# Kernel tuning notes

Hardware: AMD Instinct MI355X
Metric: run time of the kernel (lower is better)

## Reference

```python
import jax, jax.numpy as jnp
import numpy as np

C = 64
CQ = C // 8


def setup_inputs() -> dict:
    key = jax.random.key(0)
    ks = jax.random.split(key, 8)
    x = jax.random.normal(ks[0], (8, C, 64, 64), dtype=jnp.float32)
    s = 1.0 / np.sqrt(C)
    Wq = jax.random.normal(ks[1], (CQ, C), dtype=jnp.float32) * s
    bq = jax.random.normal(ks[2], (CQ,), dtype=jnp.float32) * s
    Wk = jax.random.normal(ks[3], (CQ, C), dtype=jnp.float32) * s
    bk = jax.random.normal(ks[4], (CQ,), dtype=jnp.float32) * s
    Wv = jax.random.normal(ks[5], (C, C), dtype=jnp.float32) * s
    bv = jax.random.normal(ks[6], (C,), dtype=jnp.float32) * s
    gamma = jnp.array([0.5], dtype=jnp.float32)  # nonzero so value path contributes
    return {"x": x, "Wq": Wq, "bq": bq, "Wk": Wk, "bk": bk, "Wv": Wv, "bv": bv, "gamma": gamma}


def reference(x, Wq, bq, Wk, bk, Wv, bv, gamma):
    B, Cc, H, W = x.shape
    xf = x.reshape(B, Cc, H * W)  # [B, C, N]
    # 1x1 conv == channel-mixing linear
    f = jnp.einsum('oc,bcn->bon', Wq, xf) + bq[None, :, None]  # [B, C/8, N]
    g = jnp.einsum('oc,bcn->bon', Wk, xf) + bk[None, :, None]  # [B, C/8, N]
    h = jnp.einsum('oc,bcn->bon', Wv, xf) + bv[None, :, None]  # [B, C, N]
    # scores[b,i,j] = f[b,:,i] . g[b,:,j]; softmax over dim=1 (query dim i)
    scores = jnp.einsum('bdi,bdj->bij', f, g)  # [B, N, N]
    beta = jax.nn.softmax(scores, axis=1)
    o = gamma[0] * jnp.einsum('bcn,bnm->bcm', h, beta) + xf
    return o.reshape(B, Cc, H, W)
```

## Files before the change

### kernel.cpp

```cpp
#include <hip/hip_runtime.h>
#include <hip/hip_fp16.h>


typedef _Float16 half8_t __attribute__((ext_vector_type(8)));
typedef _Float16 half4_t __attribute__((ext_vector_type(4)));
typedef _Float16 half2_t __attribute__((ext_vector_type(2)));
typedef __fp16  fp16x2  __attribute__((ext_vector_type(2)));
typedef float float4_t __attribute__((ext_vector_type(4)));

#define NTOK 4096
#define PRH 72
#define LOG2E 1.44269504088896340736f

#if __has_builtin(__builtin_amdgcn_exp2f)
__device__ __forceinline__ float fexp2(float x) { return __builtin_amdgcn_exp2f(x); }
#else
__device__ __forceinline__ float fexp2(float x) { return exp2f(x); }
#endif

__device__ __forceinline__ half2_t pkcvt(float a, float b) {
    fp16x2 v = __builtin_amdgcn_cvt_pkrtz(a, b);
    return __builtin_bit_cast(half2_t, v);
}

__global__ __launch_bounds__(320) void proj_kernel(
    const float* __restrict__ x,
    const float* __restrict__ Wq, const float* __restrict__ bq,
    const float* __restrict__ Wk, const float* __restrict__ bk,
    const float* __restrict__ Wv, const float* __restrict__ bv,
    __half* __restrict__ fTR, __half* __restrict__ gT16, __half* __restrict__ hM)
{
    __shared__ float xl[64 * 64];
    const int t  = threadIdx.x;
    const int kt = blockIdx.x;
    const int b  = blockIdx.y;
    const int n0 = kt * 64;

    if (t < 256) {
        const int f4 = t & 15;
        const int cb = t >> 4;
#pragma unroll
        for (int i = 0; i < 4; i++) {
            const int c = cb + i * 16;
            float4 v = *(const float4*)(x + (((size_t)(b * 64 + c)) << 12) + n0 + f4 * 4);
            *(float4*)(&xl[c * 64 + f4 * 4]) = v;
        }
    }
    __syncthreads();

    const int w    = t >> 6;
    const int lane = t & 63;
    const int n    = n0 + lane;
    float acc[16];

    if (w == 0) {
#pragma unroll
        for (int j = 0; j < 8; j++) { acc[j] = bq[j]; acc[8 + j] = bk[j]; }
        float xc = xl[lane];
        for (int c = 0; c < 64; c++) {
            const float xn = (c < 63) ? xl[(c + 1) * 64 + lane] : 0.f;
#pragma unroll
            for (int j = 0; j < 8; j++) {
                acc[j]     += Wq[j * 64 + c] * xc;
                acc[8 + j] += Wk[j * 64 + c] * xc;
            }
            xc = xn;
        }
        float gn2 = 0.f;
#pragma unroll
        for (int j = 0; j < 8; j++) gn2 += acc[8 + j] * acc[8 + j];
        const float M = (LOG2E * 4.6f) * __builtin_sqrtf(gn2) + 1.0f;

        const int t4 = lane >> 4, ml = lane & 15;
        half4_t flo = {(_Float16)(acc[0] * LOG2E), (_Float16)(acc[1] * LOG2E),
                       (_Float16)(acc[2] * LOG2E), (_Float16)(acc[3] * LOG2E)};
        half4_t fhi = {(_Float16)(acc[4] * LOG2E), (_Float16)(acc[5] * LOG2E),
                       (_Float16)(acc[6] * LOG2E), (_Float16)(acc[7] * LOG2E)};
        __half* fb = fTR + ((size_t)b << 15) + (size_t)(kt * 16 + ml) * 32 + t4 * 4;
        *(half4_t*)fb        = flo;
        *(half4_t*)(fb + 16) = fhi;

        half8_t glo, gpad;
#pragma unroll
        for (int j = 0; j < 8; j++) glo[j] = (_Float16)acc[8 + j];
        gpad = (half8_t){};
        gpad[0] = (_Float16)(-M);
        __half* gp = gT16 + (size_t)((b << 12) + n) * 16;
        *(half8_t*)gp       = glo;
        *(half8_t*)(gp + 8) = gpad;
    } else {
        const int ch0 = (w - 1) * 16;
#pragma unroll
        for (int j = 0; j < 16; j++) acc[j] = bv[ch0 + j];
        float xc = xl[lane];
        for (int c = 0; c < 64; c++) {
            const float xn = (c < 63) ? xl[(c + 1) * 64 + lane] : 0.f;
#pragma unroll
            for (int j = 0; j < 16; j++) acc[j] += Wv[(ch0 + j) * 64 + c] * xc;
            xc = xn;
        }
#pragma unroll
        for (int j = 0; j < 16; j++)
            hM[(((size_t)b * 64 + ch0 + j) << 12) + n] = __float2half(acc[j]);
    }
}

template<int NT>
__global__ __launch_bounds__(256) void attn_kernel(
    const __half* __restrict__ fTR, const __half* __restrict__ gT16,
    const __half* __restrict__ hM,
    __half* __restrict__ Pacc, float* __restrict__ Lsum)
{
    __shared__ __align__(16) _Float16 hl[2][64 * PRH];
    const int tid   = threadIdx.x;
    const int w     = tid >> 6;
    const int lane  = tid & 63;
    const int q     = lane >> 4;
    const int ml    = lane & 15;
    const int b     = blockIdx.y;
    const int split = blockIdx.z;
    const int colA  = blockIdx.x * 128 + w * 16 + ml;
    const int colB  = colA + 64;
    const bool qlo  = (q < 2);

    half4_t gfA = *(const half4_t*)(gT16 + ((size_t)((b << 12) + colA)) * 16 + q * 4);
    half4_t gfB = *(const half4_t*)(gT16 + ((size_t)((b << 12) + colB)) * 16 + q * 4);

    float4_t accA[4], accB[4];
#pragma unroll
    for (int cg = 0; cg < 4; cg++) {
        accA[cg] = (float4_t){0.f, 0.f, 0.f, 0.f};
        accB[cg] = (float4_t){0.f, 0.f, 0.f, 0.f};
    }
    float lsA0 = 0.f, lsA1 = 0.f, lsA2 = 0.f, lsA3 = 0.f;
    float lsB0 = 0.f, lsB1 = 0.f, lsB2 = 0.f, lsB3 = 0.f;

    const int kt0 = split * NT;
    const int c0  = tid >> 3;
    const int g0  = tid & 7;

    const __half* srow0 = hM + ((size_t)(b * 64 + c0) << 12) + kt0 * 64 + g0 * 8;
    const __half* srow1 = srow0 + ((size_t)32 << 12);
    const __half* fptr  = fTR + ((size_t)b << 15) + (size_t)(kt0 * 16 + ml) * 32 + q * 16;

    half4_t padv = (half4_t){};
    if (q == 2) padv[0] = (_Float16)1.0f;

    uint4 s0 = *(const uint4*)srow0;
    uint4 s1 = *(const uint4*)srow1;
    half4_t afn0 = padv, afn1 = padv, afn2 = padv, afn3 = padv;
    if (qlo) {
        afn0 = *(const half4_t*)(fptr);
        afn1 = *(const half4_t*)(fptr + 4);
        afn2 = *(const half4_t*)(fptr + 8);
        afn3 = *(const half4_t*)(fptr + 12);
    }
    *(uint4*)(&hl[0][c0 * PRH + g0 * 8])        = s0;
    *(uint4*)(&hl[0][(c0 + 32) * PRH + g0 * 8]) = s1;
    __syncthreads();

#pragma unroll 1
    for (int kt = 0; kt < NT; kt++) {
        const _Float16* hbL = &hl[kt & 1][ml * PRH + q * 4];

        float4_t stA0 = __builtin_amdgcn_mfma_f32_16x16x16f16(
            afn0, gfA, (float4_t){0.f, 0.f, 0.f, 0.f}, 0, 0, 0);
        float4_t stA1 = __builtin_amdgcn_mfma_f32_16x16x16f16(
            afn1, gfA, (float4_t){0.f, 0.f, 0.f, 0.f}, 0, 0, 0);
        float4_t stA2 = __builtin_amdgcn_mfma_f32_16x16x16f16(
            afn2, gfA, (float4_t){0.f, 0.f, 0.f, 0.f}, 0, 0, 0);
        float4_t stA3 = __builtin_amdgcn_mfma_f32_16x16x16f16(
            afn3, gfA, (float4_t){0.f, 0.f, 0.f, 0.f}, 0, 0, 0);
        float4_t stB0 = __builtin_amdgcn_mfma_f32_16x16x16f16(
            afn0, gfB, (float4_t){0.f, 0.f, 0.f, 0.f}, 0, 0, 0);
        float4_t stB1 = __builtin_amdgcn_mfma_f32_16x16x16f16(
            afn1, gfB, (float4_t){0.f, 0.f, 0.f, 0.f}, 0, 0, 0);
        float4_t stB2 = __builtin_amdgcn_mfma_f32_16x16x16f16(
            afn2, gfB, (float4_t){0.f, 0.f, 0.f, 0.f}, 0, 0, 0);
        float4_t stB3 = __builtin_amdgcn_mfma_f32_16x16x16f16(
            afn3, gfB, (float4_t){0.f, 0.f, 0.f, 0.f}, 0, 0, 0);

        if (kt + 1 < NT) {
            if (qlo) {
                afn0 = *(const half4_t*)(fptr + 512);
                afn1 = *(const half4_t*)(fptr + 516);
                afn2 = *(const half4_t*)(fptr + 520);
                afn3 = *(const half4_t*)(fptr + 524);
            }
            s0 = *(const uint4*)(srow0 + 64);
            s1 = *(const uint4*)(srow1 + 64);
            fptr  += 512;
            srow0 += 64;
            srow1 += 64;
        }

        {
            float pA0 = fexp2(stA0[0]), pA1 = fexp2(stA0[1]),
                  pA2 = fexp2(stA0[2]), pA3 = fexp2(stA0[3]);
            float pB0 = fexp2(stB0[0]), pB1 = fexp2(stB0[1]),
                  pB2 = fexp2(stB0[2]), pB3 = fexp2(stB0[3]);
            lsA0 += pA0; lsA1 += pA1; lsA2 += pA2; lsA3 += pA3;
            lsB0 += pB0; lsB1 += pB1; lsB2 += pB2; lsB3 += pB3;
            half2_t a_lo = pkcvt(pA0, pA1), a_hi = pkcvt(pA2, pA3);
            half2_t b_lo = pkcvt(pB0, pB1), b_hi = pkcvt(pB2, pB3);
            half4_t pfA = {a_lo[0], a_lo[1], a_hi[0], a_hi[1]};
            half4_t pfB = {b_lo[0], b_lo[1], b_hi[0], b_hi[1]};
#pragma unroll
            for (int cg = 0; cg < 4; cg++) {
                half4_t ah = *(const half4_t*)(hbL + cg * (16 * PRH) + 0 * 16);
                accA[cg] = __builtin_amdgcn_mfma_f32_16x16x16f16(ah, pfA, accA[cg], 0, 0, 0);
                accB[cg] = __builtin_amdgcn_mfma_f32_16x16x16f16(ah, pfB, accB[cg], 0, 0, 0);
            }
        }
        {
            float pA0 = fexp2(stA1[0]), pA1 = fexp2(stA1[1]),
                  pA2 = fexp2(stA1[2]), pA3 = fexp2(stA1[3]);
            float pB0 = fexp2(stB1[0]), pB1 = fexp2(stB1[1]),
                  pB2 = fexp2(stB1[2]), pB3 = fexp2(stB1[3]);
            lsA0 += pA0; lsA1 += pA1; lsA2 += pA2; lsA3 += pA3;
            lsB0 += pB0; lsB1 += pB1; lsB2 += pB2; lsB3 += pB3;
            half2_t a_lo = pkcvt(pA0, pA1), a_hi = pkcvt(pA2, pA3);
            half2_t b_lo = pkcvt(pB0, pB1), b_hi = pkcvt(pB2, pB3);
            half4_t pfA = {a_lo[0], a_lo[1], a_hi[0], a_hi[1]};
            half4_t pfB = {b_lo[0], b_lo[1], b_hi[0], b_hi[1]};
#pragma unroll
            for (int cg = 0; cg < 4; cg++) {
                half4_t ah = *(const half4_t*)(hbL + cg * (16 * PRH) + 1 * 16);
                accA[cg] = __builtin_amdgcn_mfma_f32_16x16x16f16(ah, pfA, accA[cg], 0, 0, 0);
                accB[cg] = __builtin_amdgcn_mfma_f32_16x16x16f16(ah, pfB, accB[cg], 0, 0, 0);
            }
        }
        {
            float pA0 = fexp2(stA2[0]), pA1 = fexp2(stA2[1]),
                  pA2 = fexp2(stA2[2]), pA3 = fexp2(stA2[3]);
            float pB0 = fexp2(stB2[0]), pB1 = fexp2(stB2[1]),
                  pB2 = fexp2(stB2[2]), pB3 = fexp2(stB2[3]);
            lsA0 += pA0; lsA1 += pA1; lsA2 += pA2; lsA3 += pA3;
            lsB0 += pB0; lsB1 += pB1; lsB2 += pB2; lsB3 += pB3;
            half2_t a_lo = pkcvt(pA0, pA1), a_hi = pkcvt(pA2, pA3);
            half2_t b_lo = pkcvt(pB0, pB1), b_hi = pkcvt(pB2, pB3);
            half4_t pfA = {a_lo[0], a_lo[1], a_hi[0], a_hi[1]};
            half4_t pfB = {b_lo[0], b_lo[1], b_hi[0], b_hi[1]};
#pragma unroll
            for (int cg = 0; cg < 4; cg++) {
                half4_t ah = *(const half4_t*)(hbL + cg * (16 * PRH) + 2 * 16);
                accA[cg] = __builtin_amdgcn_mfma_f32_16x16x16f16(ah, pfA, accA[cg], 0, 0, 0);
                accB[cg] = __builtin_amdgcn_mfma_f32_16x16x16f16(ah, pfB, accB[cg], 0, 0, 0);
            }
        }
        {
            float pA0 = fexp2(stA3[0]), pA1 = fexp2(stA3[1]),
                  pA2 = fexp2(stA3[2]), pA3 = fexp2(stA3[3]);
            float pB0 = fexp2(stB3[0]), pB1 = fexp2(stB3[1]),
                  pB2 = fexp2(stB3[2]), pB3 = fexp2(stB3[3]);
            lsA0 += pA0; lsA1 += pA1; lsA2 += pA2; lsA3 += pA3;
            lsB0 += pB0; lsB1 += pB1; lsB2 += pB2; lsB3 += pB3;
            half2_t a_lo = pkcvt(pA0, pA1), a_hi = pkcvt(pA2, pA3);
            half2_t b_lo = pkcvt(pB0, pB1), b_hi = pkcvt(pB2, pB3);
            half4_t pfA = {a_lo[0], a_lo[1], a_hi[0], a_hi[1]};
            half4_t pfB = {b_lo[0], b_lo[1], b_hi[0], b_hi[1]};
#pragma unroll
            for (int cg = 0; cg < 4; cg++) {
                half4_t ah = *(const half4_t*)(hbL + cg * (16 * PRH) + 3 * 16);
                accA[cg] = __builtin_amdgcn_mfma_f32_16x16x16f16(ah, pfA, accA[cg], 0, 0, 0);
                accB[cg] = __builtin_amdgcn_mfma_f32_16x16x16f16(ah, pfB, accB[cg], 0, 0, 0);
            }
        }

        if (kt + 1 < NT) {
            _Float16* hn = &hl[(kt + 1) & 1][0];
            *(uint4*)(&hn[c0 * PRH + g0 * 8])        = s0;
            *(uint4*)(&hn[(c0 + 32) * PRH + g0 * 8]) = s1;
        }
        __syncthreads();
    }

    float lA = (lsA0 + lsA1) + (lsA2 + lsA3);
    lA += __shfl_xor(lA, 16, 64);
    lA += __shfl_xor(lA, 32, 64);
    float lB = (lsB0 + lsB1) + (lsB2 + lsB3);
    lB += __shfl_xor(lB, 16, 64);
    lB += __shfl_xor(lB, 32, 64);

    __half* pa = Pacc + (((size_t)(split * 8 + b) * 64) << 12);
#pragma unroll
    for (int cg = 0; cg < 4; cg++)
#pragma unroll
        for (int r = 0; r < 4; r++) {
            int ch = cg * 16 + q * 4 + r;
            pa[((size_t)ch << 12) + colA] = __float2half(accA[cg][r]);
            pa[((size_t)ch << 12) + colB] = __float2half(accB[cg][r]);
        }
    if (q == 0) {
        Lsum[((size_t)(split * 8 + b) << 12) + colA] = lA;
        Lsum[((size_t)(split * 8 + b) << 12) + colB] = lB;
    }
}

template<int S>
__global__ __launch_bounds__(256) void merge_kernel(
    const __half* __restrict__ Pacc, const float* __restrict__ Lsum,
    const float* __restrict__ x, const float* __restrict__ gammap,
    float* __restrict__ out)
{
    __shared__ float invL[64];
    const int tid  = threadIdx.x;
    const int oc   = tid & 7;
    const int chl  = tid >> 3;
    const int b    = blockIdx.y;
    const int col0 = blockIdx.x * 64;
    const int ch   = blockIdx.z * 32 + chl;

    if (tid < 64) {
        float L = 0.f;
#pragma unroll
        for (int s = 0; s < S; s++)
            L += Lsum[((size_t)(s * 8 + b) << 12) + col0 + tid];
        invL[tid] = gammap[0] / L;
    }
    __syncthreads();

    const int cc = oc * 8;
    const size_t base = (((size_t)b * 64 + ch) << 12) + col0 + cc;
    float o[8];
#pragma unroll
    for (int i = 0; i < 8; i++) o[i] = 0.f;
#pragma unroll
    for (int s = 0; s < S; s++) {
        half8_t pv = *(const half8_t*)(Pacc +
            (((size_t)(s * 8 + b) * 64 + ch) << 12) + col0 + cc);
#pragma unroll
        for (int i = 0; i < 8; i++) o[i] += (float)pv[i];
    }
    float4 x0 = *(const float4*)(x + base);
    float4 x1 = *(const float4*)(x + base + 4);
    float4 v0, v1;
    v0.x = o[0] * invL[cc]     + x0.x;
    v0.y = o[1] * invL[cc + 1] + x0.y;
    v0.z = o[2] * invL[cc + 2] + x0.z;
    v0.w = o[3] * invL[cc + 3] + x0.w;
    v1.x = o[4] * invL[cc + 4] + x1.x;
    v1.y = o[5] * invL[cc + 5] + x1.y;
    v1.z = o[6] * invL[cc + 6] + x1.z;
    v1.w = o[7] * invL[cc + 7] + x1.w;
    *(float4*)(out + base)     = v0;
    *(float4*)(out + base + 4) = v1;
}

extern "C" void kernel_launch(void* const* d_in, const int* in_sizes, int n_in,
                              void* d_out, int out_size, void* d_ws, size_t ws_size,
                              hipStream_t stream) {
    const float* x     = (const float*)d_in[0];
    const float* Wq    = (const float*)d_in[1];
    const float* bq    = (const float*)d_in[2];
    const float* Wk    = (const float*)d_in[3];
    const float* bk    = (const float*)d_in[4];
    const float* Wv    = (const float*)d_in[5];
    const float* bv    = (const float*)d_in[6];
    const float* gamma = (const float*)d_in[7];
    float* out = (float*)d_out;

    const size_t fr_bytes  = (size_t)8 * 32768 * 2;
    const size_t g_bytes   = (size_t)8 * NTOK * 16 * 2;
    const size_t hM_bytes  = (size_t)8 * 64 * NTOK * 2;
    const size_t pa_split  = (size_t)8 * 64 * NTOK * 2;
    const size_t l_split   = (size_t)8 * NTOK * sizeof(float);
    const size_t base_need = fr_bytes + g_bytes + hM_bytes;

    int S = 1;
    if (ws_size >= base_need + 4 * (pa_split + l_split)) S = 4;
    else if (ws_size >= base_need + 2 * (pa_split + l_split)) S = 2;

    char* p = (char*)d_ws;
    __half* fTR  = (__half*)p;  p += fr_bytes;
    __half* gT16 = (__half*)p;  p += g_bytes;
    __half* hM   = (__half*)p;  p += hM_bytes;
    __half* Pacc = (__half*)p;  p += (size_t)S * pa_split;
    float*  Lsum = (float*)p;

    proj_kernel<<<dim3(64, 8), 320, 0, stream>>>(x, Wq, bq, Wk, bk, Wv, bv,
                                                 fTR, gT16, hM);
    if (S == 4) {
        attn_kernel<16><<<dim3(32, 8, 4), 256, 0, stream>>>(fTR, gT16, hM, Pacc, Lsum);
        merge_kernel<4><<<dim3(64, 8, 2), 256, 0, stream>>>(Pacc, Lsum, x, gamma, out);
    } else if (S == 2) {
        attn_kernel<32><<<dim3(32, 8, 2), 256, 0, stream>>>(fTR, gT16, hM, Pacc, Lsum);
        merge_kernel<2><<<dim3(64, 8, 2), 256, 0, stream>>>(Pacc, Lsum, x, gamma, out);
    } else {
        attn_kernel<64><<<dim3(32, 8, 1), 256, 0, stream>>>(fTR, gT16, hM, Pacc, Lsum);
        merge_kernel<1><<<dim3(64, 8, 2), 256, 0, stream>>>(Pacc, Lsum, x, gamma, out);
    }
}
```

Baseline: 136.3 us.

## Compute 1x1 conv projections with fp16 MFMA and narrow merge kernel work per thread

```diff
diff --git a/kernel.cpp b/kernel.cpp
--- a/kernel.cpp
+++ b/kernel.cpp
@@ -30,78 +30,86 @@
     const float* __restrict__ Wv, const float* __restrict__ bv,
     __half* __restrict__ fTR, __half* __restrict__ gT16, __half* __restrict__ hM)
 {
-    __shared__ float xl[64 * 64];
+    __shared__ __align__(16) _Float16 xh[64 * PRH];
     const int t  = threadIdx.x;
     const int kt = blockIdx.x;
     const int b  = blockIdx.y;
     const int n0 = kt * 64;
 
     if (t < 256) {
-        const int f4 = t & 15;
-        const int cb = t >> 4;
 #pragma unroll
         for (int i = 0; i < 4; i++) {
-            const int c = cb + i * 16;
+            const int idx = t + i * 256;
+            const int c = idx >> 4, f4 = idx & 15;
             float4 v = *(const float4*)(x + (((size_t)(b * 64 + c)) << 12) + n0 + f4 * 4);
-            *(float4*)(&xl[c * 64 + f4 * 4]) = v;
-        }
-    }
-    __syncthreads();
+            xh[(f4 * 4 + 0) * PRH + c] = (_Float16)v.x;
+            xh[(f4 * 4 + 1) * PRH + c] = (_Float16)v.y;
+            xh[(f4 * 4 + 2) * PRH + c] = (_Float16)v.z;
+            xh[(f4 * 4 + 3) * PRH + c] = (_Float16)v.w;
+        }
+    }
 
     const int w    = t >> 6;
     const int lane = t & 63;
-    const int n    = n0 + lane;
-    float acc[16];
-
-    if (w == 0) {
-#pragma unroll
-        for (int j = 0; j < 8; j++) { acc[j] = bq[j]; acc[8 + j] = bk[j]; }
-        float xc = xl[lane];
-        for (int c = 0; c < 64; c++) {
-            const float xn = (c < 63) ? xl[(c + 1) * 64 + lane] : 0.f;
-#pragma unroll
-            for (int j = 0; j < 8; j++) {
-                acc[j]     += Wq[j * 64 + c] * xc;
-                acc[8 + j] += Wk[j * 64 + c] * xc;
-            }
-            xc = xn;
-        }
-        float gn2 = 0.f;
-#pragma unroll
-        for (int j = 0; j < 8; j++) gn2 += acc[8 + j] * acc[8 + j];
-        const float M = (LOG2E * 4.6f) * __builtin_sqrtf(gn2) + 1.0f;
-
-        const int t4 = lane >> 4, ml = lane & 15;
-        half4_t flo = {(_Float16)(acc[0] * LOG2E), (_Float16)(acc[1] * LOG2E),
-                       (_Float16)(acc[2] * LOG2E), (_Float16)(acc[3] * LOG2E)};
-        half4_t fhi = {(_Float16)(acc[4] * LOG2E), (_Float16)(acc[5] * LOG2E),
-                       (_Float16)(acc[6] * LOG2E), (_Float16)(acc[7] * LOG2E)};
-        __half* fb = fTR + ((size_t)b << 15) + (size_t)(kt * 16 + ml) * 32 + t4 * 4;
-        *(half4_t*)fb        = flo;
-        *(half4_t*)(fb + 16) = fhi;
-
-        half8_t glo, gpad;
-#pragma unroll
-        for (int j = 0; j < 8; j++) glo[j] = (_Float16)acc[8 + j];
-        gpad = (half8_t){};
-        gpad[0] = (_Float16)(-M);
-        __half* gp = gT16 + (size_t)((b << 12) + n) * 16;
-        *(half8_t*)gp       = glo;
-        *(half8_t*)(gp + 8) = gpad;
-    } else {
-        const int ch0 = (w - 1) * 16;
-#pragma unroll
-        for (int j = 0; j < 16; j++) acc[j] = bv[ch0 + j];
-        float xc = xl[lane];
-        for (int c = 0; c < 64; c++) {
-            const float xn = (c < 63) ? xl[(c + 1) * 64 + lane] : 0.f;
-#pragma unroll
-            for (int j = 0; j < 16; j++) acc[j] += Wv[(ch0 + j) * 64 + c] * xc;
-            xc = xn;
-        }
-#pragma unroll
-        for (int j = 0; j < 16; j++)
-            hM[(((size_t)b * 64 + ch0 + j) << 12) + n] = __float2half(acc[j]);
+    const int q    = lane >> 4;
+    const int ml   = lane & 15;
+
+    const float* wrow;
+    if (w == 0) wrow = (ml < 8) ? (Wq + ml * 64) : (Wk + (ml - 8) * 64);
+    else        wrow = Wv + ((w - 1) * 16 + ml) * 64;
+    half4_t afr[4];
+#pragma unroll
+    for (int ks = 0; ks < 4; ks++) {
+        float4 wv4 = *(const float4*)(wrow + ks * 16 + q * 4);
+        afr[ks] = (half4_t){(_Float16)wv4.x, (_Float16)wv4.y,
+                            (_Float16)wv4.z, (_Float16)wv4.w};
+    }
+    float4 bias4;
+    if (w == 0) bias4 = (q < 2) ? *(const float4*)(bq + q * 4)
+                                : *(const float4*)(bk + (q - 2) * 4);
+    else        bias4 = *(const float4*)(bv + (w - 1) * 16 + q * 4);
+
+    __syncthreads();
+
+#pragma unroll
+    for (int cg = 0; cg < 4; cg++) {
+        float4_t acc = (float4_t){0.f, 0.f, 0.f, 0.f};
+#pragma unroll
+        for (int ks = 0; ks < 4; ks++) {
+            half4_t bfr = *(const half4_t*)(&xh[(cg * 16 + ml) * PRH + ks * 16 + q * 4]);
+            acc = __builtin_amdgcn_mfma_f32_16x16x16f16(afr[ks], bfr, acc, 0, 0, 0);
+        }
+        acc[0] += bias4.x; acc[1] += bias4.y; acc[2] += bias4.z; acc[3] += bias4.w;
+        const int tok = n0 + cg * 16 + ml;
+
+        if (w == 0) {
+            if (q < 2) {
+                half4_t fv = {(_Float16)(acc[0] * LOG2E), (_Float16)(acc[1] * LOG2E),
+                              (_Float16)(acc[2] * LOG2E), (_Float16)(acc[3] * LOG2E)};
+                *(half4_t*)(fTR + ((size_t)b << 15) +
+                            (size_t)(kt * 16 + ml) * 32 + q * 16 + cg * 4) = fv;
+            }
+            float gn2p = acc[0] * acc[0] + acc[1] * acc[1] +
+                         acc[2] * acc[2] + acc[3] * acc[3];
+            float gn2 = gn2p + __shfl_xor(gn2p, 16, 64);
+            if (q >= 2) {
+                half4_t gv = {(_Float16)acc[0], (_Float16)acc[1],
+                              (_Float16)acc[2], (_Float16)acc[3]};
+                __half* gp = gT16 + (size_t)((b << 12) + tok) * 16;
+                *(half4_t*)(gp + (q - 2) * 4) = gv;
+                if (q == 2) {
+                    const float M = (LOG2E * 4.6f) * __builtin_sqrtf(gn2) + 1.0f;
+                    *(half4_t*)(gp + 8) = (half4_t){(_Float16)(-M), 0, 0, 0};
+                } else {
+                    *(half4_t*)(gp + 12) = (half4_t){};
+                }
+            }
+        } else {
+            const int ch = (w - 1) * 16 + q * 4;
+#pragma unroll
+            for (int r = 0; r < 4; r++)
+                hM[(((size_t)b * 64 + ch + r) << 12) + tok] = __float2half(acc[r]);
+        }
     }
 }
 
@@ -305,11 +313,11 @@
 {
     __shared__ float invL[64];
     const int tid  = threadIdx.x;
-    const int oc   = tid & 7;
-    const int chl  = tid >> 3;
+    const int c4   = tid & 15;
+    const int chh  = tid >> 4;
     const int b    = blockIdx.y;
     const int col0 = blockIdx.x * 64;
-    const int ch   = blockIdx.z * 32 + chl;
+    const int ch   = blockIdx.z * 16 + chh;
 
     if (tid < 64) {
         float L = 0.f;
@@ -320,31 +328,25 @@
     }
     __syncthreads();
 
-    const int cc = oc * 8;
+    const int cc = c4 * 4;
     const size_t base = (((size_t)b * 64 + ch) << 12) + col0 + cc;
-    float o[8];
-#pragma unroll
-    for (int i = 0; i < 8; i++) o[i] = 0.f;
+    float4 xv = *(const float4*)(x + base);
+    float o0 = 0.f, o1 = 0.f, o2 = 0.f, o3 = 0.f;
 #pragma unroll
     for (int s = 0; s < S; s++) {
-        half8_t pv = *(const half8_t*)(Pacc +
+        half4_t pv = *(const half4_t*)(Pacc +
             (((size_t)(s * 8 + b) * 64 + ch) << 12) + col0 + cc);
-#pragma unroll
-        for (int i = 0; i < 8; i++) o[i] += (float)pv[i];
-    }
-    float4 x0 = *(const float4*)(x + base);
-    float4 x1 = *(const float4*)(x + base + 4);
-    float4 v0, v1;
-    v0.x = o[0] * invL[cc]     + x0.x;
-    v0.y = o[1] * invL[cc + 1] + x0.y;
-    v0.z = o[2] * invL[cc + 2] + x0.z;
-    v0.w = o[3] * invL[cc + 3] + x0.w;
-    v1.x = o[4] * invL[cc + 4] + x1.x;
-    v1.y = o[5] * invL[cc + 5] + x1.y;
-    v1.z = o[6] * invL[cc + 6] + x1.z;
-    v1.w = o[7] * invL[cc + 7] + x1.w;
-    *(float4*)(out + base)     = v0;
-    *(float4*)(out + base + 4) = v1;
+        o0 += (float)pv[0];
+        o1 += (float)pv[1];
+        o2 += (float)pv[2];
+        o3 += (float)pv[3];
+    }
+    float4 ov;
+    ov.x = o0 * invL[cc]     + xv.x;
+    ov.y = o1 * invL[cc + 1] + xv.y;
+    ov.z = o2 * invL[cc + 2] + xv.z;
+    ov.w = o3 * invL[cc + 3] + xv.w;
+    *(float4*)(out + base) = ov;
 }
 
 extern "C" void kernel_launch(void* const* d_in, const int* in_sizes, int n_in,
@@ -382,12 +384,12 @@
                                                  fTR, gT16, hM);
     if (S == 4) {
         attn_kernel<16><<<dim3(32, 8, 4), 256, 0, stream>>>(fTR, gT16, hM, Pacc, Lsum);
-        merge_kernel<4><<<dim3(64, 8, 2), 256, 0, stream>>>(Pacc, Lsum, x, gamma, out);
+        merge_kernel<4><<<dim3(64, 8, 4), 256, 0, stream>>>(Pacc, Lsum, x, gamma, out);
     } else if (S == 2) {
         attn_kernel<32><<<dim3(32, 8, 2), 256, 0, stream>>>(fTR, gT16, hM, Pacc, Lsum);
-        merge_kernel<2><<<dim3(64, 8, 2), 256, 0, stream>>>(Pacc, Lsum, x, gamma, out);
+        merge_kernel<2><<<dim3(64, 8, 4), 256, 0, stream>>>(Pacc, Lsum, x, gamma, out);
     } else {
         attn_kernel<64><<<dim3(32, 8, 1), 256, 0, stream>>>(fTR, gT16, hM, Pacc, Lsum);
-        merge_kernel<1><<<dim3(64, 8, 2), 256, 0, stream>>>(Pacc, Lsum, x, gamma, out);
-    }
-}
+        merge_kernel<1><<<dim3(64, 8, 4), 256, 0, stream>>>(Pacc, Lsum, x, gamma, out);
+    }
+}
```

New measurement: 121.3 us. -11.0%, faster.
